# Performance work log

Measured on AMD Instinct MI355X. Metric: run time of the kernel, lower is better.

Reference implementation:

```python
import jax, jax.numpy as jnp
import numpy as np

N, D, H, K, E, C = 50000, 128, 128, 5, 800000, 1


def _xavier(key, shape):
    fan_in, fan_out = shape[-2], shape[-1]
    a = (6.0 / (fan_in + fan_out)) ** 0.5
    return jax.random.uniform(key, shape, jnp.float32, -a, a)


def setup_inputs() -> dict:
    key = jax.random.key(0)
    ks = jax.random.split(key, 16)
    inp = {
        "x": jax.random.normal(ks[0], (N, D), jnp.float32),
        "edge_index_A1": jax.random.randint(ks[1], (2, E), 0, N),
        "edge_index_A2": jax.random.randint(ks[2], (2, E), 0, N),
        "edge_index_A3": jax.random.randint(ks[3], (2, E), 0, N),
        # rgcn1: 3 relation weights (D,H), linear (H,H)+bias
        "W1": _xavier(ks[4], (3, D, H)),
        "lin1_w": _xavier(ks[5], (H, H)),
        "lin1_b": jnp.zeros((H,), jnp.float32),
        # rgcn2
        "W2": _xavier(ks[6], (3, H, H)),
        "lin2_w": _xavier(ks[7], (H, H)),
        "lin2_b": jnp.zeros((H,), jnp.float32),
        # KAN layer
        "kan_w": _xavier(ks[8], (H, H)),
        "kan_b": jnp.zeros((H,), jnp.float32),
        "alpha": jnp.ones((H,), jnp.float32),
        "beta": jnp.zeros((H,), jnp.float32),
        "knots": jnp.linspace(-1.0, 1.0, K, dtype=jnp.float32),
        "spline_vals": jax.random.normal(ks[9], (H, K), jnp.float32),
        # final fc
        "fc_w": _xavier(ks[10], (C, H)),
        "fc_b": jnp.zeros((C,), jnp.float32),
    }
    return inp


def _rgcn(x, edges, Wr, lw, lb):
    # out[row] += (x @ W_r)[col], summed over relations, then linear
    out = jnp.zeros((x.shape[0], lw.shape[1]), x.dtype)
    for ei, W in zip(edges, Wr):  # fixed 3 relations
        msg = (x @ W)[ei[1]]  # gather transformed source feats
        out = out + jax.ops.segment_sum(msg, ei[0], num_segments=x.shape[0])
    return out @ lw.T + lb


def _natural_cubic_eval(knots, values, x):
    # knots (K,), values (F,K), x (N,F) -> (N,F)
    Kn = knots.shape[0]
    h = knots[1:] - knots[:-1]  # (K-1,)
    slope = (values[:, 1:] - values[:, :-1]) / h  # (F,K-1)
    rhs = 6.0 * (slope[:, 1:] - slope[:, :-1])  # (F,K-2)
    A = (jnp.diag(2.0 * (h[:-1] + h[1:]))
         + jnp.diag(h[1:-1], 1) + jnp.diag(h[1:-1], -1))
    M_inner = jnp.linalg.solve(A, rhs.T).T  # (F,K-2)
    M = jnp.pad(M_inner, ((0, 0), (1, 1)))  # natural BCs: M[0]=M[-1]=0
    j = jnp.clip(jnp.searchsorted(knots, x, side="right") - 1, 0, Kn - 2)
    f = jnp.arange(values.shape[0])[None, :]
    t0, t1 = knots[j], knots[j + 1]
    hj = t1 - t0
    y0, y1 = values[f, j], values[f, j + 1]
    M0, M1 = M[f, j], M[f, j + 1]
    a, b = t1 - x, x - t0
    return (M0 * a ** 3 / (6 * hj) + M1 * b ** 3 / (6 * hj)
            + (y0 / hj - M0 * hj / 6) * a + (y1 / hj - M1 * hj / 6) * b)


def reference(x, edge_index_A1, edge_index_A2, edge_index_A3,
              W1, lin1_w, lin1_b, W2, lin2_w, lin2_b,
              kan_w, kan_b, alpha, beta, knots, spline_vals,
              fc_w, fc_b):
    edges = (edge_index_A1, edge_index_A2, edge_index_A3)
    h1 = jax.nn.relu(_rgcn(x, edges, W1, lin1_w, lin1_b))
    h2 = jax.nn.relu(_rgcn(h1, edges, W2, lin2_w, lin2_b))
    k = alpha * (h2 @ kan_w.T + kan_b) + beta
    k = _natural_cubic_eval(knots, spline_vals, k)
    out = k @ fc_w.T + fc_b  # (N,1)
    return jnp.squeeze(out, axis=1)
```

## Files before the change

### kernel.cpp

```cpp
#include <hip/hip_runtime.h>

#define HD 128
#define EPB 4096
#define BUK 256

typedef __attribute__((ext_vector_type(8))) short bf16x8;
typedef __attribute__((ext_vector_type(4))) float f32x4;
typedef __attribute__((ext_vector_type(4))) unsigned int u32x4;

static __device__ __forceinline__ float bf2f(unsigned short u) {
    union { unsigned int i; float f; } c; c.i = ((unsigned int)u) << 16; return c.f;
}
static __device__ __forceinline__ unsigned short f2bf(float f) {
    union { float f; unsigned int i; } c; c.f = f;
    unsigned int lsb = (c.i >> 16) & 1;
    c.i += 0x7fffu + lsb;
    return (unsigned short)(c.i >> 16);
}

__global__ __launch_bounds__(256) void prep(
    const float* __restrict__ knots, const float* __restrict__ vals,
    float* __restrict__ M,
    const float* __restrict__ W1, const float* __restrict__ W2,
    const float* __restrict__ l1, const float* __restrict__ l2,
    const float* __restrict__ kw, unsigned short* __restrict__ Wt,
    const float* __restrict__ x, unsigned short* __restrict__ xb, long nxh,
    const int* __restrict__ e0, const int* __restrict__ e1,
    const int* __restrict__ e2, int* __restrict__ Hmat,
    int E, int NBLK, int NBUK, int histBase) {
    const int bid = blockIdx.x;
    const int t = threadIdx.x;
    if (bid == 0) {
        if (t < 128) {
            int f = t;
            float kn[5], v[5];
#pragma unroll
            for (int i = 0; i < 5; ++i) { kn[i] = knots[i]; v[i] = vals[f * 5 + i]; }
            float h[4], sl[4];
#pragma unroll
            for (int i = 0; i < 4; ++i) { h[i] = kn[i+1] - kn[i]; sl[i] = (v[i+1] - v[i]) / h[i]; }
            float r0 = 6.f * (sl[1] - sl[0]);
            float r1 = 6.f * (sl[2] - sl[1]);
            float r2 = 6.f * (sl[3] - sl[2]);
            float d0 = 2.f * (h[0] + h[1]), d1 = 2.f * (h[1] + h[2]), d2 = 2.f * (h[2] + h[3]);
            float e0v = h[1], e1v = h[2];
            float w1 = e0v / d0;  float d1p = d1 - w1 * e0v;  float r1p = r1 - w1 * r0;
            float w2 = e1v / d1p; float d2p = d2 - w2 * e1v;  float r2p = r2 - w2 * r1p;
            float x2 = r2p / d2p;
            float x1 = (r1p - e1v * x2) / d1p;
            float x0 = (r0 - e0v * x1) / d0;
            M[f*5+0] = 0.f; M[f*5+1] = x0; M[f*5+2] = x1; M[f*5+3] = x2; M[f*5+4] = 0.f;
        }
        return;
    }
    if (bid < 897) {
        __shared__ float Lrow[HD];
        const int id = bid - 1;
        const int mat = id >> 7, c = id & 127;
        if (mat == 6) {
            if (t < 128) Wt[(long)6 * 16384 + c * HD + t] = f2bf(kw[c * HD + t]);
            return;
        }
        const float* Wr = (mat < 3) ? (W1 + (long)mat * 16384) : (W2 + (long)(mat - 3) * 16384);
        const float* L  = (mat < 3) ? l1 : l2;
        if (t < 128) Lrow[t] = L[c * HD + t];
        __syncthreads();
        if (t < 128) {
            float s = 0.f;
#pragma unroll 8
            for (int j = 0; j < HD; ++j) s += Wr[t * HD + j] * Lrow[j];
            Wt[(long)mat * 16384 + c * HD + t] = f2bf(s);
        }
        return;
    }
    if (bid < histBase) {
        long i = ((long)(bid - 897) * 256 + t) * 8;
        if (i < nxh) {
            float4 f0 = *(const float4*)(x + i);
            float4 f1 = *(const float4*)(x + i + 4);
            ushort4 o0, o1;
            o0.x = f2bf(f0.x); o0.y = f2bf(f0.y); o0.z = f2bf(f0.z); o0.w = f2bf(f0.w);
            o1.x = f2bf(f1.x); o1.y = f2bf(f1.y); o1.z = f2bf(f1.z); o1.w = f2bf(f1.w);
            *(ushort4*)(xb + i) = o0;
            *(ushort4*)(xb + i + 4) = o1;
        }
        return;
    }
    __shared__ int hist[256];
    const int hid = bid - histBase;
    const int r = hid / NBLK, blk = hid - r * NBLK;
    const int* dst = (r == 0) ? e0 : ((r == 1) ? e1 : e2);
    if (t < NBUK) hist[t] = 0;
    __syncthreads();
    const int s0 = blk * EPB, s1 = min(s0 + EPB, E);
    for (int e = s0 + t; e < s1; e += 256) atomicAdd(&hist[dst[e] >> 8], 1);
    __syncthreads();
    if (t < NBUK) Hmat[((long)r * NBUK + t) * NBLK + blk] = hist[t];
}

template <int MODE>
__global__ __launch_bounds__(256) void mfma_gemm(
    const unsigned short* __restrict__ A, const unsigned short* __restrict__ Wt,
    void* __restrict__ Out, const float* __restrict__ bias,
    const float* __restrict__ alpha, const float* __restrict__ beta,
    const float* __restrict__ knots, const float* __restrict__ vals,
    const float* __restrict__ Msp, const float* __restrict__ fcw,
    const float* __restrict__ fcb, int n) {
    constexpr int NREL = (MODE == 1) ? 3 : 1;
    constexpr int RS   = (MODE == 1) ? 384 : 128;
    __shared__ unsigned short As[64 * HD];
    __shared__ unsigned short Ws[HD * HD];
    const int t = threadIdx.x;
    const int row0 = blockIdx.x * 64;
    const int w = t >> 6;
    const int lane = t & 63;
    const int m = lane & 15;
    const int g = lane >> 4;
    const int sw = (m & 7) << 4;

    f32x4 acc[8];
#pragma unroll
    for (int ct = 0; ct < 8; ++ct) acc[ct] = (f32x4){0.f, 0.f, 0.f, 0.f};

#pragma unroll
    for (int rel = 0; rel < NREL; ++rel) {
        if (rel) __syncthreads();
        const unsigned short* Wg = Wt + (long)rel * 16384;
        for (int i = t; i < 2048; i += 256) {
            u32x4 v = *(const u32x4*)(Wg + i * 8);
            int byte = (i * 16) ^ (((i >> 4) & 7) << 4);
            *(u32x4*)((char*)Ws + byte) = v;
        }
        for (int i = t; i < 1024; i += 256) {
            int rr = i >> 4;
            int k8 = (i & 15) << 3;
            int row = row0 + rr;
            u32x4 v = (u32x4){0u, 0u, 0u, 0u};
            if (row < n) v = *(const u32x4*)(A + (long)row * RS + rel * HD + k8);
            int byte = (i * 16) ^ ((rr & 7) << 4);
            *(u32x4*)((char*)As + byte) = v;
        }
        __syncthreads();
#pragma unroll
        for (int ks = 0; ks < 4; ++ks) {
            const int kb = ks * 64 + g * 16;
            bf16x8 af = *(const bf16x8*)((const char*)As + ((((w * 16 + m) << 8) + kb) ^ sw));
#pragma unroll
            for (int ct = 0; ct < 8; ++ct) {
                bf16x8 bf = *(const bf16x8*)((const char*)Ws + ((((ct * 16 + m) << 8) + kb) ^ sw));
                acc[ct] = __builtin_amdgcn_mfma_f32_16x16x32_bf16(af, bf, acc[ct], 0, 0, 0);
            }
        }
    }

    if (MODE == 1) {
        unsigned short* C = (unsigned short*)Out;
#pragma unroll
        for (int ct = 0; ct < 8; ++ct) {
            float bv = bias[ct * 16 + m];
#pragma unroll
            for (int r = 0; r < 4; ++r) {
                int row = row0 + w * 16 + g * 4 + r;
                if (row < n)
                    C[(long)row * HD + ct * 16 + m] = f2bf(fmaxf(acc[ct][r] + bv, 0.f));
            }
        }
    } else {
        float kn[5];
#pragma unroll
        for (int i = 0; i < 5; ++i) kn[i] = knots[i];
        float part[4] = {0.f, 0.f, 0.f, 0.f};
#pragma unroll
        for (int ct = 0; ct < 8; ++ct) {
            int f = ct * 16 + m;
            float kb = bias[f], al = alpha[f], be = beta[f], fw = fcw[f];
#pragma unroll
            for (int r = 0; r < 4; ++r) {
                float xv = al * (acc[ct][r] + kb) + be;
                int j = -1;
#pragma unroll
                for (int k = 0; k < 5; ++k) j += (xv >= kn[k]) ? 1 : 0;
                j = max(0, min(3, j));
                float t0 = kn[j], t1 = kn[j + 1];
                float hj = t1 - t0;
                float y0 = vals[f * 5 + j], y1 = vals[f * 5 + j + 1];
                float M0 = Msp[f * 5 + j], M1 = Msp[f * 5 + j + 1];
                float a = t1 - xv, b = xv - t0;
                float inv6h = 1.f / (6.f * hj);
                float s = M0 * a * a * a * inv6h + M1 * b * b * b * inv6h
                        + (y0 / hj - M0 * hj / 6.f) * a + (y1 / hj - M1 * hj / 6.f) * b;
                part[r] += s * fw;
            }
        }
#pragma unroll
        for (int o = 1; o < 16; o <<= 1) {
#pragma unroll
            for (int r = 0; r < 4; ++r) part[r] += __shfl_xor(part[r], o);
        }
        if (m == 0) {
#pragma unroll
            for (int r = 0; r < 4; ++r) {
                int row = row0 + w * 16 + g * 4 + r;
                if (row < n) ((float*)Out)[row] = part[r] + fcb[0];
            }
        }
    }
}

__global__ __launch_bounds__(256) void scanA(const int* __restrict__ cnt,
                                             int* __restrict__ S,
                                             int* __restrict__ bsum, int n) {
    __shared__ int ts[256];
    const int t = threadIdx.x;
    const int base = blockIdx.x * 2048 + t * 8;
    int v[8];
    int s = 0;
#pragma unroll
    for (int i = 0; i < 8; ++i) {
        int j = base + i;
        v[i] = (j < n) ? cnt[j] : 0;
        s += v[i];
    }
    ts[t] = s;
    __syncthreads();
    for (int off = 1; off < 256; off <<= 1) {
        int x = (t >= off) ? ts[t - off] : 0;
        __syncthreads();
        ts[t] += x;
        __syncthreads();
    }
    int excl = ts[t] - s;
#pragma unroll
    for (int i = 0; i < 8; ++i) {
        int j = base + i;
        if (j < n) S[j] = excl;
        excl += v[i];
    }
    if (t == 255) bsum[blockIdx.x] = ts[255];
}

__global__ __launch_bounds__(256) void scanC(int* __restrict__ S,
                                             const int* __restrict__ bsum,
                                             int n, int total) {
    __shared__ int red[256];
    const int t = threadIdx.x;
    int acc = 0;
    for (int b = t; b < blockIdx.x; b += 256) acc += bsum[b];
    red[t] = acc;
    __syncthreads();
    for (int o = 128; o; o >>= 1) {
        if (t < o) red[t] += red[t + o];
        __syncthreads();
    }
    const int off = red[0];
    const int base = blockIdx.x * 2048 + t * 8;
#pragma unroll
    for (int i = 0; i < 8; ++i) {
        int j = base + i;
        if (j < n) S[j] += off;
    }
    if (blockIdx.x == gridDim.x - 1 && t == 0) S[n] = total;
}

__global__ __launch_bounds__(256) void fill_pass(
    const int* __restrict__ e0, const int* __restrict__ e1,
    const int* __restrict__ e2, const int* __restrict__ O,
    unsigned int* __restrict__ P, int E, int NBLK, int NBUK) {
    __shared__ int cur[256];
    const int r = blockIdx.y, blk = blockIdx.x, t = threadIdx.x;
    const int* eb = (r == 0) ? e0 : ((r == 1) ? e1 : e2);
    if (t < NBUK) cur[t] = O[((long)r * NBUK + t) * NBLK + blk];
    __syncthreads();
    const int s0 = blk * EPB, s1 = min(s0 + EPB, E);
    for (int e = s0 + t; e < s1; e += 256) {
        int dst = eb[e], src = eb[E + e];
        int pos = atomicAdd(&cur[dst >> 8], 1);
        P[pos] = ((unsigned)(dst & 255) << 16) | (unsigned)src;
    }
}

__global__ __launch_bounds__(256) void bucket_scatter2(
    const unsigned int* __restrict__ P, const int* __restrict__ O,
    unsigned short* __restrict__ srcs, int* __restrict__ S,
    int N, int NBUK, int NBLK, int E3) {
    __shared__ int cnt[256], pos[256], cur[256];
    const int b = blockIdx.x, r = blockIdx.y, t = threadIdx.x;
    const int d0 = b * BUK;
    const long oidx = (long)r * NBUK + b;
    const int pb = O[oidx * NBLK];
    const int pe = (oidx + 1 < (long)3 * NBUK) ? O[(oidx + 1) * NBLK] : E3;
    cnt[t] = 0;
    __syncthreads();
    for (int i = pb + t; i < pe; i += 256) atomicAdd(&cnt[P[i] >> 16], 1);
    __syncthreads();
    int v = cnt[t];
    pos[t] = v;
    __syncthreads();
    for (int off = 1; off < 256; off <<= 1) {
        int x = (t >= off) ? pos[t - off] : 0;
        __syncthreads();
        pos[t] += x;
        __syncthreads();
    }
    int start = pb + pos[t] - v;
    cur[t] = start;
    int d = d0 + t;
    if (d < N) S[(long)r * N + d] = start;
    __syncthreads();
    for (int i = pb + t; i < pe; i += 256) {
        unsigned pk = P[i];
        int p2 = atomicAdd(&cur[pk >> 16], 1);
        srcs[p2] = (unsigned short)(pk & 0xFFFFu);
    }
    if (b == NBUK - 1 && r == 2 && t == 0) S[(long)3 * N] = E3;
}

__global__ __launch_bounds__(256) void csr_agg3(const unsigned short* __restrict__ X,
                                                const int* __restrict__ S,
                                                const unsigned short* __restrict__ srcs,
                                                unsigned short* __restrict__ Ag, int N) {
    const int g = threadIdx.x >> 4;
    const int lane = threadIdx.x & 15;
    const int d = blockIdx.x * 16 + g;
    if (d >= N) return;
    const unsigned short* Xb = X + lane * 8;
#pragma unroll
    for (int r = 0; r < 3; ++r) {
        const int beg = S[(long)r * N + d];
        const int end = S[(long)r * N + d + 1];
        float ac[8] = {0.f, 0.f, 0.f, 0.f, 0.f, 0.f, 0.f, 0.f};
        int e = beg;
        for (; e + 7 < end; e += 8) {
            u32x4 v0 = *(const u32x4*)(Xb + (long)srcs[e    ] * HD);
            u32x4 v1 = *(const u32x4*)(Xb + (long)srcs[e + 1] * HD);
            u32x4 v2 = *(const u32x4*)(Xb + (long)srcs[e + 2] * HD);
            u32x4 v3 = *(const u32x4*)(Xb + (long)srcs[e + 3] * HD);
            u32x4 v4 = *(const u32x4*)(Xb + (long)srcs[e + 4] * HD);
            u32x4 v5 = *(const u32x4*)(Xb + (long)srcs[e + 5] * HD);
            u32x4 v6 = *(const u32x4*)(Xb + (long)srcs[e + 6] * HD);
            u32x4 v7 = *(const u32x4*)(Xb + (long)srcs[e + 7] * HD);
#pragma unroll
            for (int c = 0; c < 4; ++c) {
                ac[2*c]   += bf2f((unsigned short)(v0[c] & 0xffff)) + bf2f((unsigned short)(v1[c] & 0xffff))
                           + bf2f((unsigned short)(v2[c] & 0xffff)) + bf2f((unsigned short)(v3[c] & 0xffff))
                           + bf2f((unsigned short)(v4[c] & 0xffff)) + bf2f((unsigned short)(v5[c] & 0xffff))
                           + bf2f((unsigned short)(v6[c] & 0xffff)) + bf2f((unsigned short)(v7[c] & 0xffff));
                ac[2*c+1] += bf2f((unsigned short)(v0[c] >> 16)) + bf2f((unsigned short)(v1[c] >> 16))
                           + bf2f((unsigned short)(v2[c] >> 16)) + bf2f((unsigned short)(v3[c] >> 16))
                           + bf2f((unsigned short)(v4[c] >> 16)) + bf2f((unsigned short)(v5[c] >> 16))
                           + bf2f((unsigned short)(v6[c] >> 16)) + bf2f((unsigned short)(v7[c] >> 16));
            }
        }
        for (; e < end; ++e) {
            u32x4 v0 = *(const u32x4*)(Xb + (long)srcs[e] * HD);
#pragma unroll
            for (int c = 0; c < 4; ++c) {
                ac[2*c]   += bf2f((unsigned short)(v0[c] & 0xffff));
                ac[2*c+1] += bf2f((unsigned short)(v0[c] >> 16));
            }
        }
        ushort4 o0, o1;
        o0.x = f2bf(ac[0]); o0.y = f2bf(ac[1]); o0.z = f2bf(ac[2]); o0.w = f2bf(ac[3]);
        o1.x = f2bf(ac[4]); o1.y = f2bf(ac[5]); o1.z = f2bf(ac[6]); o1.w = f2bf(ac[7]);
        unsigned short* Op = &Ag[(long)d * 384 + r * HD + lane * 8];
        *(ushort4*)Op = o0;
        *(ushort4*)(Op + 4) = o1;
    }
}

extern "C" void kernel_launch(void* const* d_in, const int* in_sizes, int n_in,
                              void* d_out, int out_size, void* d_ws, size_t ws_size,
                              hipStream_t stream) {
    const float* x       = (const float*)d_in[0];
    const int*   eA[3]   = {(const int*)d_in[1], (const int*)d_in[2], (const int*)d_in[3]};
    const float* W1      = (const float*)d_in[4];
    const float* lin1_w  = (const float*)d_in[5];
    const float* lin1_b  = (const float*)d_in[6];
    const float* W2      = (const float*)d_in[7];
    const float* lin2_w  = (const float*)d_in[8];
    const float* lin2_b  = (const float*)d_in[9];
    const float* kan_w   = (const float*)d_in[10];
    const float* kan_b   = (const float*)d_in[11];
    const float* alpha   = (const float*)d_in[12];
    const float* beta    = (const float*)d_in[13];
    const float* knots   = (const float*)d_in[14];
    const float* spline_vals = (const float*)d_in[15];
    const float* fc_w    = (const float*)d_in[16];
    const float* fc_b    = (const float*)d_in[17];

    const int N = in_sizes[0] / HD;
    const int E = in_sizes[1] / 2;
    const int NBUK = (N + BUK - 1) / BUK;
    const int NBLK = (E + EPB - 1) / EPB;
    const int nH   = 3 * NBUK * NBLK;

    char* p = (char*)d_ws;
    auto carve = [&](size_t bytes) {
        char* q = p;
        p += (bytes + 255) & ~(size_t)255;
        return q;
    };
    float* M              = (float*)carve(4096);
    unsigned short* Wt    = (unsigned short*)carve((size_t)7 * 16384 * 2);
    int* Hmat             = (int*)carve((size_t)nH * 4);
    int* O                = (int*)carve((size_t)(nH + 1) * 4);
    int* bsum             = (int*)carve(4096);
    int* S                = (int*)carve((size_t)(3 * N + 1) * 4);
    unsigned int* P       = (unsigned int*)carve((size_t)3 * E * 4);
    unsigned short* srcs  = (unsigned short*)carve((size_t)3 * E * 2);
    unsigned short* xb    = (unsigned short*)carve((size_t)N * HD * 2);
    unsigned short* hb    = (unsigned short*)carve((size_t)N * HD * 2);
    unsigned short* Ag    = (unsigned short*)carve((size_t)N * 384 * 2);

    const long nxh = (long)N * HD;
    const int xcastB = (int)((nxh + 2047) / 2048);
    const int histBase = 1 + 896 + xcastB;
    const int prepGrid = histBase + 3 * NBLK;
    const int g64      = (N + 63) / 64;
    const int aggGrid  = (N + 15) / 16;
    const int scanGrid = (nH + 2047) / 2048;

    prep<<<prepGrid, 256, 0, stream>>>(knots, spline_vals, M, W1, W2, lin1_w, lin2_w,
                                       kan_w, Wt, x, xb, nxh,
                                       eA[0], eA[1], eA[2], Hmat, E, NBLK, NBUK, histBase);

    scanA<<<scanGrid, 256, 0, stream>>>(Hmat, O, bsum, nH);
    scanC<<<scanGrid, 256, 0, stream>>>(O, bsum, nH, 3 * E);
    fill_pass<<<dim3(NBLK, 3), 256, 0, stream>>>(eA[0], eA[1], eA[2], O, P, E, NBLK, NBUK);
    bucket_scatter2<<<dim3(NBUK, 3), 256, 0, stream>>>(P, O, srcs, S, N, NBUK, NBLK, 3 * E);

    csr_agg3<<<aggGrid, 256, 0, stream>>>(xb, S, srcs, Ag, N);
    mfma_gemm<1><<<g64, 256, 0, stream>>>(Ag, Wt, hb, lin1_b, nullptr, nullptr,
                                          nullptr, nullptr, nullptr, nullptr, nullptr, N);

    csr_agg3<<<aggGrid, 256, 0, stream>>>(hb, S, srcs, Ag, N);
    mfma_gemm<1><<<g64, 256, 0, stream>>>(Ag, Wt + (size_t)3 * 16384, hb, lin2_b, nullptr,
                                          nullptr, nullptr, nullptr, nullptr, nullptr, nullptr, N);

    mfma_gemm<2><<<g64, 256, 0, stream>>>(hb, Wt + (size_t)6 * 16384, d_out, kan_b, alpha,
                                          beta, knots, spline_vals, M, fc_w, fc_b, N);
}
```

Baseline: 298.9 us.

## Fuse second RGCN GEMM with KAN spline GEMM and use nontemporal loads/stores

The second relational GEMM and the KAN/spline/fc GEMM are merged into one kernel. The ReLU'd h2 tile is written to shared memory as bf16 and multiplied by the KAN weights in place, so the h2 round-trip through global memory and one launch are removed. The aggregation output now uses a packed 128-bit nontemporal store, and the GEMM A loads are nontemporal to limit cache pollution. The fused kernel keeps the relation loop fixed at 3, so MODE 2 can no longer be instantiated. It also adds an extra LDS pass and sync per block.

```diff
diff --git a/kernel.cpp b/kernel.cpp
--- a/kernel.cpp
+++ b/kernel.cpp
@@ -101,13 +101,13 @@
 template <int MODE>
 __global__ __launch_bounds__(256) void mfma_gemm(
     const unsigned short* __restrict__ A, const unsigned short* __restrict__ Wt,
+    const unsigned short* __restrict__ Wt2,
     void* __restrict__ Out, const float* __restrict__ bias,
+    const float* __restrict__ bias2,
     const float* __restrict__ alpha, const float* __restrict__ beta,
     const float* __restrict__ knots, const float* __restrict__ vals,
     const float* __restrict__ Msp, const float* __restrict__ fcw,
     const float* __restrict__ fcb, int n) {
-    constexpr int NREL = (MODE == 1) ? 3 : 1;
-    constexpr int RS   = (MODE == 1) ? 384 : 128;
     __shared__ unsigned short As[64 * HD];
     __shared__ unsigned short Ws[HD * HD];
     const int t = threadIdx.x;
@@ -123,7 +123,7 @@
     for (int ct = 0; ct < 8; ++ct) acc[ct] = (f32x4){0.f, 0.f, 0.f, 0.f};
 
 #pragma unroll
-    for (int rel = 0; rel < NREL; ++rel) {
+    for (int rel = 0; rel < 3; ++rel) {
         if (rel) __syncthreads();
         const unsigned short* Wg = Wt + (long)rel * 16384;
         for (int i = t; i < 2048; i += 256) {
@@ -136,7 +136,7 @@
             int k8 = (i & 15) << 3;
             int row = row0 + rr;
             u32x4 v = (u32x4){0u, 0u, 0u, 0u};
-            if (row < n) v = *(const u32x4*)(A + (long)row * RS + rel * HD + k8);
+            if (row < n) v = __builtin_nontemporal_load((const u32x4*)(A + (long)row * 384 + rel * HD + k8));
             int byte = (i * 16) ^ ((rr & 7) << 4);
             *(u32x4*)((char*)As + byte) = v;
         }
@@ -166,6 +166,36 @@
             }
         }
     } else {
+        __syncthreads();
+#pragma unroll
+        for (int ct = 0; ct < 8; ++ct) {
+            float bv = bias[ct * 16 + m];
+#pragma unroll
+            for (int r = 0; r < 4; ++r) {
+                int row = w * 16 + g * 4 + r;
+                float hv = fmaxf(acc[ct][r] + bv, 0.f);
+                int byte = ((row << 8) + ((ct * 16 + m) << 1)) ^ ((row & 7) << 4);
+                *(unsigned short*)((char*)As + byte) = f2bf(hv);
+            }
+        }
+        for (int i = t; i < 2048; i += 256) {
+            u32x4 v = *(const u32x4*)(Wt2 + i * 8);
+            int byte = (i * 16) ^ (((i >> 4) & 7) << 4);
+            *(u32x4*)((char*)Ws + byte) = v;
+        }
+        __syncthreads();
+#pragma unroll
+        for (int ct = 0; ct < 8; ++ct) acc[ct] = (f32x4){0.f, 0.f, 0.f, 0.f};
+#pragma unroll
+        for (int ks = 0; ks < 4; ++ks) {
+            const int kb = ks * 64 + g * 16;
+            bf16x8 af = *(const bf16x8*)((const char*)As + ((((w * 16 + m) << 8) + kb) ^ sw));
+#pragma unroll
+            for (int ct = 0; ct < 8; ++ct) {
+                bf16x8 bf = *(const bf16x8*)((const char*)Ws + ((((ct * 16 + m) << 8) + kb) ^ sw));
+                acc[ct] = __builtin_amdgcn_mfma_f32_16x16x32_bf16(af, bf, acc[ct], 0, 0, 0);
+            }
+        }
         float kn[5];
 #pragma unroll
         for (int i = 0; i < 5; ++i) kn[i] = knots[i];
@@ -173,7 +203,7 @@
 #pragma unroll
         for (int ct = 0; ct < 8; ++ct) {
             int f = ct * 16 + m;
-            float kb = bias[f], al = alpha[f], be = beta[f], fw = fcw[f];
+            float kb = bias2[f], al = alpha[f], be = beta[f], fw = fcw[f];
 #pragma unroll
             for (int r = 0; r < 4; ++r) {
                 float xv = al * (acc[ct][r] + kb) + be;
@@ -359,12 +389,12 @@
                 ac[2*c+1] += bf2f((unsigned short)(v0[c] >> 16));
             }
         }
-        ushort4 o0, o1;
-        o0.x = f2bf(ac[0]); o0.y = f2bf(ac[1]); o0.z = f2bf(ac[2]); o0.w = f2bf(ac[3]);
-        o1.x = f2bf(ac[4]); o1.y = f2bf(ac[5]); o1.z = f2bf(ac[6]); o1.w = f2bf(ac[7]);
-        unsigned short* Op = &Ag[(long)d * 384 + r * HD + lane * 8];
-        *(ushort4*)Op = o0;
-        *(ushort4*)(Op + 4) = o1;
+        u32x4 ov;
+        ov[0] = (unsigned)f2bf(ac[0]) | ((unsigned)f2bf(ac[1]) << 16);
+        ov[1] = (unsigned)f2bf(ac[2]) | ((unsigned)f2bf(ac[3]) << 16);
+        ov[2] = (unsigned)f2bf(ac[4]) | ((unsigned)f2bf(ac[5]) << 16);
+        ov[3] = (unsigned)f2bf(ac[6]) | ((unsigned)f2bf(ac[7]) << 16);
+        __builtin_nontemporal_store(ov, (u32x4*)&Ag[(long)d * 384 + r * HD + lane * 8]);
     }
 }
 
@@ -430,13 +460,13 @@
     bucket_scatter2<<<dim3(NBUK, 3), 256, 0, stream>>>(P, O, srcs, S, N, NBUK, NBLK, 3 * E);
 
     csr_agg3<<<aggGrid, 256, 0, stream>>>(xb, S, srcs, Ag, N);
-    mfma_gemm<1><<<g64, 256, 0, stream>>>(Ag, Wt, hb, lin1_b, nullptr, nullptr,
-                                          nullptr, nullptr, nullptr, nullptr, nullptr, N);
+    mfma_gemm<1><<<g64, 256, 0, stream>>>(Ag, Wt, nullptr, hb, lin1_b, nullptr,
+                                          nullptr, nullptr, nullptr, nullptr,
+                                          nullptr, nullptr, nullptr, N);
 
     csr_agg3<<<aggGrid, 256, 0, stream>>>(hb, S, srcs, Ag, N);
-    mfma_gemm<1><<<g64, 256, 0, stream>>>(Ag, Wt + (size_t)3 * 16384, hb, lin2_b, nullptr,
-                                          nullptr, nullptr, nullptr, nullptr, nullptr, nullptr, N);
-
-    mfma_gemm<2><<<g64, 256, 0, stream>>>(hb, Wt + (size_t)6 * 16384, d_out, kan_b, alpha,
-                                          beta, knots, spline_vals, M, fc_w, fc_b, N);
-}
+    mfma_gemm<3><<<g64, 256, 0, stream>>>(Ag, Wt + (size_t)3 * 16384,
+                                          Wt + (size_t)6 * 16384, d_out, lin2_b, kan_b,
+                                          alpha, beta, knots, spline_vals, M,
+                                          fc_w, fc_b, N);
+}
```

Measured after the change: 286.3 us (median of 2 runs). 1.04x faster.
